# Performance work log

Hardware: AMD Instinct MI355X
Metric: run time of the kernel (lower is better)

Reference implementation:

```python
import jax, jax.numpy as jnp
import numpy as np

H = 8          # n_heads
MRF = 128      # max_rf random features
EPS = 1e-4


def fiber2head(feats, h):
    # feats: list of [N, m_d, 2d+1] -> [N, h, sum_d (m_d/h)*(2d+1)]
    N = feats[0].shape[0]
    return jnp.concatenate([f.reshape(N, h, -1) for f in feats], axis=-1)


def softmax_kernel(data, w, is_query):
    # FAVOR+ positive random features. data: [B,H,L,d], w: [m,d]
    dn = data.shape[-1] ** -0.25
    ratio = w.shape[0] ** -0.5
    dd = jnp.einsum('bhld,md->bhlm', data * dn, w)
    diag = (data * data).sum(-1, keepdims=True) * (0.5 * dn * dn)
    if is_query:
        mx = jax.lax.stop_gradient(dd.max(-1, keepdims=True))
    else:
        mx = jax.lax.stop_gradient(dd.max())
    return ratio * (jnp.exp(dd - diag - mx) + EPS)


def setup_inputs() -> dict:
    key = jax.random.key(0)
    ks = jax.random.split(key, 7)
    B, L = 4, 8192
    N = B * L
    v0 = jax.random.normal(ks[0], (N, 64, 1), jnp.float32)
    v1 = jax.random.normal(ks[1], (N, 64, 3), jnp.float32)
    k0 = jax.random.normal(ks[2], (N, 64, 1), jnp.float32)
    k1 = jax.random.normal(ks[3], (N, 64, 3), jnp.float32)
    q0 = jax.random.normal(ks[4], (N, 64, 1), jnp.float32)
    q1 = jax.random.normal(ks[5], (N, 64, 3), jnp.float32)
    w = jax.random.normal(ks[6], (MRF, 32), jnp.float32)  # random-feature projection
    return {'v0': v0, 'v1': v1, 'k0': k0, 'k1': k1, 'q0': q0, 'q1': q1, 'w': w, 'batch_size': 4}


def reference(v0, v1, k0, k1, q0, q1, w, batch_size):
    B = batch_size
    N = v0.shape[0]
    L = N // B
    # Q from the k-dict (as in source); source then overwrites K with Q, so the
    # q-dict features are mathematically unused.
    Q = fiber2head([k0, k1], H).reshape(B, L, H, -1).transpose(0, 2, 1, 3)  # [B,H,L,d_k]
    K = Q  # faithful to `K = Q.view(...)` in the source
    Kp = softmax_kernel(K, w, is_query=False)  # [B,H,L,m]
    Qp = softmax_kernel(Q, w, is_query=True)   # [B,H,L,m]
    # Normalizer is identical for every value channel (q/k are expanded copies).
    D_inv = 1.0 / jnp.einsum('bhlm,bhm->bhl', Qp, Kp.sum(axis=2))
    outs = []
    for v in (v0, v1):
        m, e = v.shape[1], v.shape[2]     # multiplicity, 2d+1
        c = m // H                         # channels per head
        vv = v.reshape(B, L, H, c, e).transpose(0, 2, 3, 1, 4)  # [B,H,c,L,e]
        # linear attention: context [B,H,c,m,e] is small -> O(L*m*e) traffic
        ctx = jnp.einsum('bhlm,bhcle->bhcme', Kp, vv)
        o = jnp.einsum('bhcme,bhlm,bhl->bhcle', ctx, Qp, D_inv)
        o = o.reshape(B, H * c, L, e).transpose(0, 2, 1, 3).reshape(B * L, c * H, e)
        outs.append(o)
    return tuple(outs)  # (out_deg0 [N,64,1], out_deg1 [N,64,3])
```

## Files before the change

### kernel.cpp

```cpp
#include <hip/hip_runtime.h>

#define BB 4
#define HH 8
#define LL 8192
#define NN (BB*LL)
#define DDIM 32
#define MM 128

#define CTXR_OFF 0
#define KSUMR_OFF (CTXR_OFF + 32*8*MM*4)
#define VSUM_OFF  (KSUMR_OFF + 32*MM)
#define GMAX_OFF  (VSUM_OFF + 32*32)
#define ZERO_FLOATS (GMAX_OFF + 1)

#define DN 0.42044820762685725f
#define RATIO 0.08838834764831845f
#define EPSF 1e-4f

#define ACC_UPDATE(kp, a0, a1, b4)                                     \
    do {                                                               \
        acc[0]  = fmaf(kp,(a0).x,acc[0]);   acc[4]  = fmaf(kp,(a0).y,acc[4]);  \
        acc[8]  = fmaf(kp,(a0).z,acc[8]);   acc[12] = fmaf(kp,(a0).w,acc[12]); \
        acc[16] = fmaf(kp,(a1).x,acc[16]);  acc[20] = fmaf(kp,(a1).y,acc[20]); \
        acc[24] = fmaf(kp,(a1).z,acc[24]);  acc[28] = fmaf(kp,(a1).w,acc[28]); \
        float4 g;                                                      \
        g = (b4)[0];                                                   \
        acc[1]=fmaf(kp,g.x,acc[1]);  acc[2]=fmaf(kp,g.y,acc[2]);       \
        acc[3]=fmaf(kp,g.z,acc[3]);  acc[5]=fmaf(kp,g.w,acc[5]);       \
        g = (b4)[1];                                                   \
        acc[6]=fmaf(kp,g.x,acc[6]);  acc[7]=fmaf(kp,g.y,acc[7]);       \
        acc[9]=fmaf(kp,g.z,acc[9]);  acc[10]=fmaf(kp,g.w,acc[10]);     \
        g = (b4)[2];                                                   \
        acc[11]=fmaf(kp,g.x,acc[11]); acc[13]=fmaf(kp,g.y,acc[13]);    \
        acc[14]=fmaf(kp,g.z,acc[14]); acc[15]=fmaf(kp,g.w,acc[15]);    \
        g = (b4)[3];                                                   \
        acc[17]=fmaf(kp,g.x,acc[17]); acc[18]=fmaf(kp,g.y,acc[18]);    \
        acc[19]=fmaf(kp,g.z,acc[19]); acc[21]=fmaf(kp,g.w,acc[21]);    \
        g = (b4)[4];                                                   \
        acc[22]=fmaf(kp,g.x,acc[22]); acc[23]=fmaf(kp,g.y,acc[23]);    \
        acc[25]=fmaf(kp,g.z,acc[25]); acc[26]=fmaf(kp,g.w,acc[26]);    \
        g = (b4)[5];                                                   \
        acc[27]=fmaf(kp,g.x,acc[27]); acc[29]=fmaf(kp,g.y,acc[29]);    \
        acc[30]=fmaf(kp,g.z,acc[30]); acc[31]=fmaf(kp,g.w,acc[31]);    \
    } while (0)

__global__ __launch_bounds__(256, 2) void k_ctx1(const float* __restrict__ kk0,
                                                 const float* __restrict__ kk1,
                                                 const float* __restrict__ v0,
                                                 const float* __restrict__ v1,
                                                 const float* __restrict__ w,
                                                 float* __restrict__ ws) {
    __shared__ float red[2][64][34];
    const int tid = threadIdx.x;
    const int lane = tid & 63;
    const int wid  = __builtin_amdgcn_readfirstlane(tid >> 6);
    const int half = wid & 1, rgrp = wid >> 1;
    const int m = half*64 + lane;
    const int bh = blockIdx.x >> 5, chunk = blockIdx.x & 31;
    const int b = bh >> 3, h = bh & 7;
    const int n0 = b*LL + chunk*256 + rgrp*128;
    float wreg[32];
    {
        const float4* w4 = (const float4*)(w + m*DDIM);
#pragma unroll
        for (int q = 0; q < 8; ++q) {
            const float4 t = w4[q];
            wreg[q*4+0]=t.x*DN; wreg[q*4+1]=t.y*DN;
            wreg[q*4+2]=t.z*DN; wreg[q*4+3]=t.w*DN;
        }
    }
    float acc[32];
#pragma unroll
    for (int i = 0; i < 32; ++i) acc[i] = 0.f;
    float ksum_acc = 0.f, vsum_acc = 0.f, wmax = -3.4e38f;
    for (int s = 0; s < 8; ++s) {
        const int nb = n0 + s*16;
        const int dr_ = lane >> 2, dq = lane & 3;
        float diagv;
        {
            const int n = nb + dr_;
            float4 da, db;
            if (dq == 0) {
                da = *(const float4*)(kk0 + (size_t)n*64 + h*8);
                db = *(const float4*)(kk0 + (size_t)n*64 + h*8 + 4);
            } else {
                const float* bp = kk1 + (size_t)n*192 + h*24 + (dq-1)*8;
                da = *(const float4*)bp; db = *(const float4*)(bp + 4);
            }
            float ss = da.x*da.x+da.y*da.y+da.z*da.z+da.w*da.w
                     + db.x*db.x+db.y*db.y+db.z*db.z+db.w*db.w;
            ss += __shfl_xor(ss, 1); ss += __shfl_xor(ss, 2);
            diagv = 0.5f*DN*DN*ss;
        }
        if (half == 0) {
            const int ve = lane & 31, vg = lane >> 5;
#pragma unroll
            for (int rr = 0; rr < 8; ++rr) {
                const int n = nb + vg*8 + rr;
                vsum_acc += (ve < 8) ? v0[(size_t)n*64 + h*8 + ve]
                                     : v1[(size_t)n*192 + h*24 + (ve-8)];
            }
        }
#pragma unroll 1
        for (int r = 0; r < 16; r += 2) {
            const int nA = nb + r, nB = nb + r + 1;
            const float dgA = __uint_as_float(
                __builtin_amdgcn_readlane(__float_as_uint(diagv), r*4));
            const float dgB = __uint_as_float(
                __builtin_amdgcn_readlane(__float_as_uint(diagv), r*4 + 4));
            float4 kA[8], kB[8];
            kA[0] = *(const float4*)(kk0 + (size_t)nA*64 + h*8);
            kA[1] = *(const float4*)(kk0 + (size_t)nA*64 + h*8 + 4);
            kB[0] = *(const float4*)(kk0 + (size_t)nB*64 + h*8);
            kB[1] = *(const float4*)(kk0 + (size_t)nB*64 + h*8 + 4);
            {
                const float4* gA4 = (const float4*)(kk1 + (size_t)nA*192 + h*24);
                const float4* gB4 = (const float4*)(kk1 + (size_t)nB*192 + h*24);
#pragma unroll
                for (int gq = 0; gq < 6; ++gq) { kA[2+gq] = gA4[gq]; kB[2+gq] = gB4[gq]; }
            }
            float ddA0 = 0.f, ddA1 = 0.f, ddB0 = 0.f, ddB1 = 0.f;
#pragma unroll
            for (int q = 0; q < 8; ++q) {
                ddA0 = fmaf(kA[q].x, wreg[q*4+0], ddA0);
                ddB0 = fmaf(kB[q].x, wreg[q*4+0], ddB0);
                ddA1 = fmaf(kA[q].y, wreg[q*4+1], ddA1);
                ddB1 = fmaf(kB[q].y, wreg[q*4+1], ddB1);
                ddA0 = fmaf(kA[q].z, wreg[q*4+2], ddA0);
                ddB0 = fmaf(kB[q].z, wreg[q*4+2], ddB0);
                ddA1 = fmaf(kA[q].w, wreg[q*4+3], ddA1);
                ddB1 = fmaf(kB[q].w, wreg[q*4+3], ddB1);
            }
            const float ddA = ddA0 + ddA1;
            const float ddB = ddB0 + ddB1;
            wmax = fmaxf(wmax, fmaxf(ddA, ddB));
            const float kpA = __expf(ddA - dgA);
            const float kpB = __expf(ddB - dgB);
            ksum_acc += kpA; ksum_acc += kpB;
            const float4 aA0 = *(const float4*)(v0 + (size_t)nA*64 + h*8);
            const float4 aA1 = *(const float4*)(v0 + (size_t)nA*64 + h*8 + 4);
            const float4 aB0 = *(const float4*)(v0 + (size_t)nB*64 + h*8);
            const float4 aB1 = *(const float4*)(v0 + (size_t)nB*64 + h*8 + 4);
            const float4* bA4 = (const float4*)(v1 + (size_t)nA*192 + h*24);
            const float4* bB4 = (const float4*)(v1 + (size_t)nB*192 + h*24);
            ACC_UPDATE(kpA, aA0, aA1, bA4);
            ACC_UPDATE(kpB, aB0, aB1, bB4);
        }
    }
    if (rgrp == 1) {
#pragma unroll
        for (int i = 0; i < 32; ++i) red[half][lane][i] = acc[i];
        red[half][lane][32] = ksum_acc;
        red[half][lane][33] = vsum_acc;
    }
    __syncthreads();
    if (rgrp == 0) {
#pragma unroll
        for (int i = 0; i < 32; ++i) acc[i] += red[half][lane][i];
        ksum_acc += red[half][lane][32];
        vsum_acc += red[half][lane][33];
        float* ctxr = ws + CTXR_OFF;
#pragma unroll
        for (int c = 0; c < 8; ++c)
#pragma unroll
            for (int j = 0; j < 4; ++j)
                atomicAdd(&ctxr[((bh*8 + c)*MM + m)*4 + j], acc[c*4+j]);
        atomicAdd(ws + KSUMR_OFF + bh*MM + m, ksum_acc);
        if (half == 0) {
            const int ve = lane & 31;
            const int packed = (ve < 8) ? ve*4
                                        : ((ve-8)/3)*4 + 1 + (ve-8)%3;
            atomicAdd(ws + VSUM_OFF + bh*32 + packed, vsum_acc);
        }
    }
#pragma unroll
    for (int off = 32; off; off >>= 1) wmax = fmaxf(wmax, __shfl_xor(wmax, off, 64));
    if (lane == 0) {
        unsigned u = __float_as_uint(wmax);
        u = (u & 0x80000000u) ? ~u : (u | 0x80000000u);
        atomicMax((unsigned*)(ws + GMAX_OFF), u);
    }
}

__global__ __launch_bounds__(256, 1) void k_out(const float* __restrict__ kk0,
                                                const float* __restrict__ kk1,
                                                const float* __restrict__ w,
                                                const float* __restrict__ ws,
                                                float* __restrict__ out) {
    __shared__ float ctx_s[128*36];
    __shared__ float wlds[128*36];
    __shared__ float ksl[128];
    __shared__ __align__(16) float sS0[32];
    __shared__ float sK0;
    const int tid = threadIdx.x;
    const int bh = blockIdx.x >> 4, chunk = blockIdx.x & 15;
    const int b = bh >> 3, h = bh & 7;
    const unsigned gu = *((const unsigned*)(ws + GMAX_OFF));
    const float gm = (gu & 0x80000000u) ? __uint_as_float(gu & 0x7fffffffu)
                                        : __uint_as_float(~gu);
    const float alpha = __expf(-gm);
    const float4* ctxr4 = (const float4*)(ws + CTXR_OFF) + (size_t)bh*1024;
    const float* vsg = ws + VSUM_OFF + bh*32;
#pragma unroll
    for (int it = 0; it < 4; ++it) {
        const int i = tid + it*256;
        const int c = i >> 7, mm2 = i & 127;
        const float4 q = ctxr4[i];
        const int p0 = c*4;
        ctx_s[mm2*36+p0+0] = RATIO*(alpha*q.x + EPSF*vsg[p0+0]);
        ctx_s[mm2*36+p0+1] = RATIO*(alpha*q.y + EPSF*vsg[p0+1]);
        ctx_s[mm2*36+p0+2] = RATIO*(alpha*q.z + EPSF*vsg[p0+2]);
        ctx_s[mm2*36+p0+3] = RATIO*(alpha*q.w + EPSF*vsg[p0+3]);
    }
    {
        const float4* w4 = (const float4*)w;
#pragma unroll
        for (int it = 0; it < 4; ++it) {
            const int i = tid + it*256;
            const int mm2 = i >> 3, q = i & 7;
            float4 t = w4[i];
            t.x*=DN; t.y*=DN; t.z*=DN; t.w*=DN;
            *(float4*)&wlds[mm2*36+q*4] = t;
        }
    }
    if (tid < 128) ksl[tid] = RATIO*(alpha*ws[KSUMR_OFF + bh*MM + tid] + EPSF*(float)LL);
    __syncthreads();
    if (tid < 32) {
        float s = 0.f;
#pragma unroll 8
        for (int mm2 = 0; mm2 < 128; ++mm2) s += ctx_s[mm2*36 + tid];
        sS0[tid] = s;
    } else if (tid < 64) {
        const int p2 = tid - 32;
        float s = ksl[p2] + ksl[32+p2] + ksl[64+p2] + ksl[96+p2];
        s += __shfl_xor(s, 1); s += __shfl_xor(s, 2); s += __shfl_xor(s, 4);
        s += __shfl_xor(s, 8); s += __shfl_xor(s, 16);
        if (p2 == 0) sK0 = s;
    }
    __syncthreads();
    const int nA = b*LL + chunk*512 + tid;
    const int nB = nA + 256;
    float KA[32], KB[32];
    {
        const float4 f0 = *(const float4*)(kk0 + (size_t)nA*64 + h*8);
        const float4 f1 = *(const float4*)(kk0 + (size_t)nA*64 + h*8 + 4);
        KA[0]=f0.x; KA[1]=f0.y; KA[2]=f0.z; KA[3]=f0.w;
        KA[4]=f1.x; KA[5]=f1.y; KA[6]=f1.z; KA[7]=f1.w;
        const float4 g0 = *(const float4*)(kk0 + (size_t)nB*64 + h*8);
        const float4 g1 = *(const float4*)(kk0 + (size_t)nB*64 + h*8 + 4);
        KB[0]=g0.x; KB[1]=g0.y; KB[2]=g0.z; KB[3]=g0.w;
        KB[4]=g1.x; KB[5]=g1.y; KB[6]=g1.z; KB[7]=g1.w;
        const float4* a4 = (const float4*)(kk1 + (size_t)nA*192 + h*24);
        const float4* b4 = (const float4*)(kk1 + (size_t)nB*192 + h*24);
#pragma unroll
        for (int gq = 0; gq < 6; ++gq) {
            const float4 ga = a4[gq];
            KA[8+gq*4+0]=ga.x; KA[8+gq*4+1]=ga.y; KA[8+gq*4+2]=ga.z; KA[8+gq*4+3]=ga.w;
            const float4 gb = b4[gq];
            KB[8+gq*4+0]=gb.x; KB[8+gq*4+1]=gb.y; KB[8+gq*4+2]=gb.z; KB[8+gq*4+3]=gb.w;
        }
    }
    float dgA = 0.f, dgB = 0.f;
#pragma unroll
    for (int d = 0; d < 32; ++d) { dgA = fmaf(KA[d], KA[d], dgA); dgB = fmaf(KB[d], KB[d], dgB); }
    dgA *= 0.5f*DN*DN;  dgB *= 0.5f*DN*DN;
    float S1A[32], S1B[32];
#pragma unroll
    for (int i = 0; i < 32; ++i) { S1A[i] = 0.f; S1B[i] = 0.f; }
    float denA = 0.f, denB = 0.f, mxA = -3.4e38f, mxB = -3.4e38f;
#pragma unroll 1
    for (int m2 = 0; m2 < 128; ++m2) {
        const float* wrow = &wlds[m2*36];
        float dA0 = 0.f, dA1 = 0.f, dB0 = 0.f, dB1 = 0.f;
#pragma unroll
        for (int q = 0; q < 8; ++q) {
            const float4 wv = *(const float4*)&wrow[q*4];
            dA0 = fmaf(KA[q*4+0], wv.x, dA0);
            dB0 = fmaf(KB[q*4+0], wv.x, dB0);
            dA1 = fmaf(KA[q*4+1], wv.y, dA1);
            dB1 = fmaf(KB[q*4+1], wv.y, dB1);
            dA0 = fmaf(KA[q*4+2], wv.z, dA0);
            dB0 = fmaf(KB[q*4+2], wv.z, dB0);
            dA1 = fmaf(KA[q*4+3], wv.w, dA1);
            dB1 = fmaf(KB[q*4+3], wv.w, dB1);
        }
        const float ddA = dA0 + dA1;
        const float ddB = dB0 + dB1;
        mxA = fmaxf(mxA, ddA);
        mxB = fmaxf(mxB, ddB);
        const float EA = __expf(ddA - dgA);
        const float EB = __expf(ddB - dgB);
        denA = fmaf(EA, ksl[m2], denA);
        denB = fmaf(EB, ksl[m2], denB);
        const float* crow = &ctx_s[m2*36];
#pragma unroll
        for (int q = 0; q < 8; ++q) {
            const float4 cv = *(const float4*)&crow[q*4];
            S1A[q*4+0] = fmaf(EA, cv.x, S1A[q*4+0]);
            S1B[q*4+0] = fmaf(EB, cv.x, S1B[q*4+0]);
            S1A[q*4+1] = fmaf(EA, cv.y, S1A[q*4+1]);
            S1B[q*4+1] = fmaf(EB, cv.y, S1B[q*4+1]);
            S1A[q*4+2] = fmaf(EA, cv.z, S1A[q*4+2]);
            S1B[q*4+2] = fmaf(EB, cv.z, S1B[q*4+2]);
            S1A[q*4+3] = fmaf(EA, cv.w, S1A[q*4+3]);
            S1B[q*4+3] = fmaf(EB, cv.w, S1B[q*4+3]);
        }
    }
    const float esA = __expf(-mxA);
    const float esB = __expf(-mxB);
    const float dinvA = 1.f / fmaf(esA, denA, EPSF*sK0);
    const float dinvB = 1.f / fmaf(esB, denB, EPSF*sK0);
    float vA[32], vB[32];
#pragma unroll
    for (int q = 0; q < 8; ++q) {
        const float4 s0 = *(const float4*)&sS0[q*4];
        vA[q*4+0] = fmaf(esA, S1A[q*4+0], EPSF*s0.x)*dinvA;
        vA[q*4+1] = fmaf(esA, S1A[q*4+1], EPSF*s0.y)*dinvA;
        vA[q*4+2] = fmaf(esA, S1A[q*4+2], EPSF*s0.z)*dinvA;
        vA[q*4+3] = fmaf(esA, S1A[q*4+3], EPSF*s0.w)*dinvA;
        vB[q*4+0] = fmaf(esB, S1B[q*4+0], EPSF*s0.x)*dinvB;
        vB[q*4+1] = fmaf(esB, S1B[q*4+1], EPSF*s0.y)*dinvB;
        vB[q*4+2] = fmaf(esB, S1B[q*4+2], EPSF*s0.z)*dinvB;
        vB[q*4+3] = fmaf(esB, S1B[q*4+3], EPSF*s0.w)*dinvB;
    }
    {
        float* o0 = out + (size_t)nA*64 + h*8;
        *(float4*)(o0)     = make_float4(vA[0],  vA[4],  vA[8],  vA[12]);
        *(float4*)(o0 + 4) = make_float4(vA[16], vA[20], vA[24], vA[28]);
        float* o1 = out + (size_t)NN*64 + (size_t)nA*192 + h*24;
        *(float4*)(o1 +  0) = make_float4(vA[1],  vA[2],  vA[3],  vA[5]);
        *(float4*)(o1 +  4) = make_float4(vA[6],  vA[7],  vA[9],  vA[10]);
        *(float4*)(o1 +  8) = make_float4(vA[11], vA[13], vA[14], vA[15]);
        *(float4*)(o1 + 12) = make_float4(vA[17], vA[18], vA[19], vA[21]);
        *(float4*)(o1 + 16) = make_float4(vA[22], vA[23], vA[25], vA[26]);
        *(float4*)(o1 + 20) = make_float4(vA[27], vA[29], vA[30], vA[31]);
    }
    {
        float* o0 = out + (size_t)nB*64 + h*8;
        *(float4*)(o0)     = make_float4(vB[0],  vB[4],  vB[8],  vB[12]);
        *(float4*)(o0 + 4) = make_float4(vB[16], vB[20], vB[24], vB[28]);
        float* o1 = out + (size_t)NN*64 + (size_t)nB*192 + h*24;
        *(float4*)(o1 +  0) = make_float4(vB[1],  vB[2],  vB[3],  vB[5]);
        *(float4*)(o1 +  4) = make_float4(vB[6],  vB[7],  vB[9],  vB[10]);
        *(float4*)(o1 +  8) = make_float4(vB[11], vB[13], vB[14], vB[15]);
        *(float4*)(o1 + 12) = make_float4(vB[17], vB[18], vB[19], vB[21]);
        *(float4*)(o1 + 16) = make_float4(vB[22], vB[23], vB[25], vB[26]);
        *(float4*)(o1 + 20) = make_float4(vB[27], vB[29], vB[30], vB[31]);
    }
}

extern "C" void kernel_launch(void* const* d_in, const int* in_sizes, int n_in,
                              void* d_out, int out_size, void* d_ws, size_t ws_size,
                              hipStream_t stream) {
    const float* v0 = (const float*)d_in[0];
    const float* v1 = (const float*)d_in[1];
    const float* k0 = (const float*)d_in[2];
    const float* k1 = (const float*)d_in[3];
    const float* w  = (const float*)d_in[6];
    float* out = (float*)d_out;
    float* ws  = (float*)d_ws;
    hipMemsetAsync(ws, 0, (size_t)ZERO_FLOATS*sizeof(float), stream);
    k_ctx1<<<1024, 256, 0, stream>>>(k0, k1, v0, v1, w, ws);
    k_out <<<512, 256, 0, stream>>>(k0, k1, w, ws, out);
}
```

Before: 216.2 us.

## Split random-feature halves across blocks and four row groups per block in k_ctx1

```diff
diff --git a/kernel.cpp b/kernel.cpp
--- a/kernel.cpp
+++ b/kernel.cpp
@@ -53,12 +53,13 @@
     __shared__ float red[2][64][34];
     const int tid = threadIdx.x;
     const int lane = tid & 63;
-    const int wid  = __builtin_amdgcn_readfirstlane(tid >> 6);
-    const int half = wid & 1, rgrp = wid >> 1;
-    const int m = half*64 + lane;
-    const int bh = blockIdx.x >> 5, chunk = blockIdx.x & 31;
+    const int wv  = __builtin_amdgcn_readfirstlane(tid >> 6);
+    const int bh = blockIdx.x >> 6;
+    const int chunk = (blockIdx.x >> 1) & 31;
+    const int mhalf = blockIdx.x & 1;
+    const int m = mhalf*64 + lane;
     const int b = bh >> 3, h = bh & 7;
-    const int n0 = b*LL + chunk*256 + rgrp*128;
+    const int n0 = b*LL + chunk*256 + wv*64;
     float wreg[32];
     {
         const float4* w4 = (const float4*)(w + m*DDIM);
@@ -73,7 +74,7 @@
 #pragma unroll
     for (int i = 0; i < 32; ++i) acc[i] = 0.f;
     float ksum_acc = 0.f, vsum_acc = 0.f, wmax = -3.4e38f;
-    for (int s = 0; s < 8; ++s) {
+    for (int s = 0; s < 4; ++s) {
         const int nb = n0 + s*16;
         const int dr_ = lane >> 2, dq = lane & 3;
         float diagv;
@@ -92,7 +93,7 @@
             ss += __shfl_xor(ss, 1); ss += __shfl_xor(ss, 2);
             diagv = 0.5f*DN*DN*ss;
         }
-        if (half == 0) {
+        if (mhalf == 0) {
             const int ve = lane & 31, vg = lane >> 5;
 #pragma unroll
             for (int rr = 0; rr < 8; ++rr) {
@@ -147,18 +148,34 @@
             ACC_UPDATE(kpB, aB0, aB1, bB4);
         }
     }
-    if (rgrp == 1) {
-#pragma unroll
-        for (int i = 0; i < 32; ++i) red[half][lane][i] = acc[i];
-        red[half][lane][32] = ksum_acc;
-        red[half][lane][33] = vsum_acc;
-    }
-    __syncthreads();
-    if (rgrp == 0) {
-#pragma unroll
-        for (int i = 0; i < 32; ++i) acc[i] += red[half][lane][i];
-        ksum_acc += red[half][lane][32];
-        vsum_acc += red[half][lane][33];
+    if (wv == 1 || wv == 3) {
+        float (*rp)[34] = red[wv >> 1];
+#pragma unroll
+        for (int i = 0; i < 32; ++i) rp[lane][i] = acc[i];
+        rp[lane][32] = ksum_acc;
+        rp[lane][33] = vsum_acc;
+    }
+    __syncthreads();
+    if (wv == 0 || wv == 2) {
+        float (*rp)[34] = red[wv >> 1];
+#pragma unroll
+        for (int i = 0; i < 32; ++i) acc[i] += rp[lane][i];
+        ksum_acc += rp[lane][32];
+        vsum_acc += rp[lane][33];
+    }
+    __syncthreads();
+    if (wv == 2) {
+#pragma unroll
+        for (int i = 0; i < 32; ++i) red[0][lane][i] = acc[i];
+        red[0][lane][32] = ksum_acc;
+        red[0][lane][33] = vsum_acc;
+    }
+    __syncthreads();
+    if (wv == 0) {
+#pragma unroll
+        for (int i = 0; i < 32; ++i) acc[i] += red[0][lane][i];
+        ksum_acc += red[0][lane][32];
+        vsum_acc += red[0][lane][33];
         float* ctxr = ws + CTXR_OFF;
 #pragma unroll
         for (int c = 0; c < 8; ++c)
@@ -166,7 +183,7 @@
             for (int j = 0; j < 4; ++j)
                 atomicAdd(&ctxr[((bh*8 + c)*MM + m)*4 + j], acc[c*4+j]);
         atomicAdd(ws + KSUMR_OFF + bh*MM + m, ksum_acc);
-        if (half == 0) {
+        if (mhalf == 0) {
             const int ve = lane & 31;
             const int packed = (ve < 8) ? ve*4
                                         : ((ve-8)/3)*4 + 1 + (ve-8)%3;
@@ -360,6 +377,6 @@
     float* out = (float*)d_out;
     float* ws  = (float*)d_ws;
     hipMemsetAsync(ws, 0, (size_t)ZERO_FLOATS*sizeof(float), stream);
-    k_ctx1<<<1024, 256, 0, stream>>>(k0, k1, v0, v1, w, ws);
+    k_ctx1<<<2048, 256, 0, stream>>>(k0, k1, v0, v1, w, ws);
     k_out <<<512, 256, 0, stream>>>(k0, k1, w, ws, out);
 }
```

Result: slower. 259.9 us (+20.2%).
